# Optimization experiments

Hardware: AMD Instinct MI355X
Metric: run time of the kernel (lower is better)

## Reference

```python
import jax, jax.numpy as jnp
import numpy as np

B, S, H, K = 64, 512, 1024, 7

def setup_inputs() -> dict:
    key = jax.random.key(0)
    ks = jax.random.split(key, 7)
    x = jax.random.normal(ks[0], (B, S, H), dtype=jnp.float32)
    gt = jax.random.randint(ks[1], (B, S), 0, K, dtype=jnp.int64)
    mask = jnp.ones((B, S), dtype=bool)
    # learned parameters
    W = jax.random.normal(ks[2], (H, K), dtype=jnp.float32) * (1.0 / np.sqrt(H))
    b = jnp.zeros((K,), dtype=jnp.float32)
    start_trans = jax.random.uniform(ks[3], (K,), minval=-0.1, maxval=0.1)
    end_trans = jax.random.uniform(ks[4], (K,), minval=-0.1, maxval=0.1)
    trans = jax.random.uniform(ks[5], (K, K), minval=-0.1, maxval=0.1)
    return {"x": x, "gt": gt, "mask": mask, "W": W, "b": b,
            "start_trans": start_trans, "end_trans": end_trans, "trans": trans}

def _crf_neg_llh(emissions, gt, mask, start_trans, end_trans, trans):
    # emissions: [B,S,K], gt: [B,S] int, mask: [B,S] bool
    maskf = mask.astype(emissions.dtype)
    # ---- numerator: score of gold path ----
    em_at_tag = jnp.take_along_axis(emissions, gt[..., None], axis=-1)[..., 0]  # [B,S]
    trans_sc = trans[gt[:, :-1], gt[:, 1:]]                                      # [B,S-1]
    num = start_trans[gt[:, 0]] + em_at_tag[:, 0]
    num = num + jnp.sum((trans_sc + em_at_tag[:, 1:]) * maskf[:, 1:], axis=1)
    last_idx = jnp.sum(mask, axis=1).astype(jnp.int32) - 1                       # [B]
    last_tags = jnp.take_along_axis(gt, last_idx[:, None], axis=1)[:, 0]
    num = num + end_trans[last_tags]
    # ---- denominator: log partition via forward algorithm (lax.scan) ----
    alpha0 = start_trans[None, :] + emissions[:, 0]                              # [B,K]
    em_rest = jnp.transpose(emissions[:, 1:], (1, 0, 2))                         # [S-1,B,K]
    m_rest = jnp.transpose(mask[:, 1:], (1, 0))                                  # [S-1,B]
    def step(alpha, inp):
        em_t, m_t = inp
        nxt = jax.nn.logsumexp(alpha[:, :, None] + trans[None, :, :] + em_t[:, None, :], axis=1)
        return jnp.where(m_t[:, None], nxt, alpha), None
    alpha, _ = jax.lax.scan(step, alpha0, (em_rest, m_rest))
    denom = jax.nn.logsumexp(alpha + end_trans[None, :], axis=1)                 # [B]
    llh = num - denom
    return -jnp.mean(llh)  # reduction='mean', module returns negative

def reference(x, gt, mask, W, b, start_trans, end_trans, trans):
    emissions = jnp.einsum('bsh,hk->bsk', x, W) + b
    return _crf_neg_llh(emissions, gt, mask, start_trans, end_trans, trans)
```

## Files before the change

kernel.cpp:

```cpp
#include <hip/hip_runtime.h>
#include <math.h>

#define NB 64
#define NS 512
#define NH 1024
#define NK 7
#define NCHUNK 16
#define CLEN 32

__global__ __launch_bounds__(256) void emis_kernel(
    const float* __restrict__ x, const float* __restrict__ W,
    const float* __restrict__ bias, float* __restrict__ em, int nrows)
{
    const int lane    = threadIdx.x & 63;
    const int wave_id = blockIdx.x * (blockDim.x >> 6) + (threadIdx.x >> 6);
    const int nwaves  = gridDim.x * (blockDim.x >> 6);

    float w[4][4][NK];
#pragma unroll
    for (int c = 0; c < 4; ++c)
#pragma unroll
        for (int i = 0; i < 4; ++i) {
            const int h = 4 * (c * 64 + lane) + i;
#pragma unroll
            for (int k = 0; k < NK; ++k)
                w[c][i][k] = W[h * NK + k];
        }
    const float bl = bias[lane < NK ? lane : 0];

    for (int row = wave_id; row < nrows; row += nwaves) {
        const float4* xr = (const float4*)(x + (size_t)row * NH);
        float acc[NK];
#pragma unroll
        for (int k = 0; k < NK; ++k) acc[k] = 0.f;
#pragma unroll
        for (int c = 0; c < 4; ++c) {
            const float4 v = xr[c * 64 + lane];
#pragma unroll
            for (int k = 0; k < NK; ++k)
                acc[k] += v.x * w[c][0][k] + v.y * w[c][1][k]
                        + v.z * w[c][2][k] + v.w * w[c][3][k];
        }
#pragma unroll
        for (int m = 1; m < 8; m <<= 1)
#pragma unroll
            for (int k = 0; k < NK; ++k)
                acc[k] += __shfl_xor(acc[k], m, 64);
        const int s = lane & 7;
        const float v01 = (s & 1) ? acc[1] : acc[0];
        const float v23 = (s & 1) ? acc[3] : acc[2];
        const float v45 = (s & 1) ? acc[5] : acc[4];
        const float v67 = acc[6];
        const float w03 = (s & 2) ? v23 : v01;
        const float w47 = (s & 2) ? v67 : v45;
        float v = (s & 4) ? w47 : w03;
        v += __shfl_xor(v, 8, 64);
        v += __shfl_xor(v, 16, 64);
        v += __shfl_xor(v, 32, 64);
        if (lane < NK)
            em[(size_t)row * NK + lane] = v + bl;
    }
}

__global__ __launch_bounds__(64) void chunk_kernel(
    const float* __restrict__ em, const float* __restrict__ trans,
    float* __restrict__ chunkP)
{
    __shared__ float lds_em[CLEN * 8];
    __shared__ float lds_tr[49];
    const int lane = threadIdx.x;
    const int b = blockIdx.x >> 4;
    const int c = blockIdx.x & (NCHUNK - 1);
    const int t0 = c * CLEN;

    if (lane < 49) lds_tr[lane] = trans[lane];
    const float* emb = em + ((size_t)b * NS + t0) * NK;
    for (int idx = lane; idx < CLEN * NK; idx += 64) {
        const int t = idx / NK;
        const int k = idx - t * NK;
        lds_em[t * 8 + k] = emb[idx];
    }
    __syncthreads();

    const int li = lane < 49 ? lane : 48;
    const int i = li / 7;
    const int k = li - i * 7;
    float tj[NK];
#pragma unroll
    for (int j = 0; j < NK; ++j) tj[j] = lds_tr[j * 7 + k];

    const int ts = (c == 0) ? 1 : t0;
    float P = lds_tr[i * 7 + k] + lds_em[(ts - t0) * 8 + k];
    for (int t = ts + 1; t < t0 + CLEN; ++t) {
        float a[NK];
#pragma unroll
        for (int j = 0; j < NK; ++j)
            a[j] = __shfl(P, i * 7 + j, 64) + tj[j];
        const float m = fmaxf(fmaxf(fmaxf(a[0], a[1]), fmaxf(a[2], a[3])),
                              fmaxf(fmaxf(a[4], a[5]), a[6]));
        const float su = __expf(a[0]-m) + __expf(a[1]-m) + __expf(a[2]-m)
                       + __expf(a[3]-m) + __expf(a[4]-m) + __expf(a[5]-m)
                       + __expf(a[6]-m);
        P = m + __logf(su) + lds_em[(t - t0) * 8 + k];
    }
    if (lane < 49)
        chunkP[(size_t)(b * NCHUNK + c) * 49 + lane] = P;
}

__global__ __launch_bounds__(64) void combine_kernel(
    const float* __restrict__ em, const float* __restrict__ chunkP,
    const int* __restrict__ gt32,
    const float* __restrict__ start_trans, const float* __restrict__ end_trans,
    const float* __restrict__ trans, float* __restrict__ llh_out)
{
    __shared__ float lds_C[NCHUNK * 49];
    __shared__ float lds_tr[49];
    __shared__ int   lds_gt[NS];
    const int b    = blockIdx.x;
    const int lane = threadIdx.x;

    int oddbits = 0;
    for (int i = lane; i < 256; i += 64) oddbits |= gt32[2 * i + 1];
    const bool is64 = (__ballot(oddbits != 0) == 0ull);

    for (int idx = lane; idx < NCHUNK * 49; idx += 64)
        lds_C[idx] = chunkP[(size_t)b * NCHUNK * 49 + idx];
    for (int i = lane; i < NS; i += 64) {
        const int gidx = b * NS + i;
        lds_gt[i] = is64 ? gt32[2 * gidx] : gt32[gidx];
    }
    if (lane < 49) lds_tr[lane] = trans[lane];
    __syncthreads();

    const float* emb = em + (size_t)b * NS * NK;
    float numpart = 0.f;
#pragma unroll
    for (int ii = 0; ii < NS / 64; ++ii) {
        const int t = lane + 64 * ii;
        const int g = lds_gt[t];
        if (t == 0) numpart += start_trans[g] + emb[g];
        else        numpart += lds_tr[lds_gt[t - 1] * 7 + g] + emb[t * NK + g];
    }
#pragma unroll
    for (int m = 1; m < 64; m <<= 1) numpart += __shfl_xor(numpart, m, 64);
    const float num = numpart + end_trans[lds_gt[NS - 1]];

    const int kk = lane < NK ? lane : NK - 1;
    float alpha = start_trans[kk] + emb[kk];
#pragma unroll
    for (int c = 0; c < NCHUNK; ++c) {
        float a[NK];
#pragma unroll
        for (int j = 0; j < NK; ++j)
            a[j] = __shfl(alpha, j, 64) + lds_C[c * 49 + j * 7 + kk];
        const float m = fmaxf(fmaxf(fmaxf(a[0], a[1]), fmaxf(a[2], a[3])),
                              fmaxf(fmaxf(a[4], a[5]), a[6]));
        const float su = __expf(a[0]-m) + __expf(a[1]-m) + __expf(a[2]-m)
                       + __expf(a[3]-m) + __expf(a[4]-m) + __expf(a[5]-m)
                       + __expf(a[6]-m);
        alpha = m + __logf(su);
    }

    float v = (lane < NK) ? (alpha + end_trans[kk]) : -3.0e38f;
    float mv = v;
#pragma unroll
    for (int m = 1; m < 8; m <<= 1) mv = fmaxf(mv, __shfl_xor(mv, m, 64));
    float e = (lane < NK) ? __expf(v - mv) : 0.f;
#pragma unroll
    for (int m = 1; m < 8; m <<= 1) e += __shfl_xor(e, m, 64);
    if (lane == 0) llh_out[b] = (mv + __logf(e)) - num;
}

__global__ __launch_bounds__(64) void reduce_kernel(
    const float* __restrict__ llh, float* __restrict__ out)
{
    float v = llh[threadIdx.x];
#pragma unroll
    for (int m = 1; m < 64; m <<= 1) v += __shfl_xor(v, m, 64);
    if (threadIdx.x == 0) out[0] = v * (1.0f / NB);
}

extern "C" void kernel_launch(void* const* d_in, const int* in_sizes, int n_in,
                              void* d_out, int out_size, void* d_ws, size_t ws_size,
                              hipStream_t stream)
{
    const float* x    = (const float*)d_in[0];
    const int*   gt   = (const int*)d_in[1];
    const float* W    = (const float*)d_in[3];
    const float* bias = (const float*)d_in[4];
    const float* st   = (const float*)d_in[5];
    const float* et   = (const float*)d_in[6];
    const float* tr   = (const float*)d_in[7];

    float* em     = (float*)d_ws;
    float* chunkP = em + (size_t)NB * NS * NK;
    float* llh    = chunkP + (size_t)NB * NCHUNK * 49;

    emis_kernel<<<512, 256, 0, stream>>>(x, W, bias, em, NB * NS);
    chunk_kernel<<<NB * NCHUNK, 64, 0, stream>>>(em, tr, chunkP);
    combine_kernel<<<NB, 64, 0, stream>>>(em, chunkP, gt, st, et, tr, llh);
    reduce_kernel<<<1, 64, 0, stream>>>(llh, (float*)d_out);
}
```

Measured before the change: 227.5 us.

## Fuse emission GEMV into chunk scan and fold mean via atomicAdd

```diff
diff --git a/kernel.cpp b/kernel.cpp
--- a/kernel.cpp
+++ b/kernel.cpp
@@ -8,38 +8,47 @@
 #define NCHUNK 16
 #define CLEN 32
 
-__global__ __launch_bounds__(256) void emis_kernel(
+__global__ __launch_bounds__(256) void fused_emis_chunk(
     const float* __restrict__ x, const float* __restrict__ W,
-    const float* __restrict__ bias, float* __restrict__ em, int nrows)
+    const float* __restrict__ bias, const float* __restrict__ trans,
+    float* __restrict__ em, float* __restrict__ chunkP)
 {
-    const int lane    = threadIdx.x & 63;
-    const int wave_id = blockIdx.x * (blockDim.x >> 6) + (threadIdx.x >> 6);
-    const int nwaves  = gridDim.x * (blockDim.x >> 6);
+    __shared__ float lds_em[CLEN * 8];
+    __shared__ float lds_tr[49];
+
+    const int lane = threadIdx.x & 63;
+    const int wave = threadIdx.x >> 6;
+    const int b = blockIdx.x >> 4;
+    const int c = blockIdx.x & (NCHUNK - 1);
+    const int t0 = c * CLEN;
+    const int row0 = b * NS + t0;
+
+    if (threadIdx.x < 49) lds_tr[threadIdx.x] = trans[threadIdx.x];
 
     float w[4][4][NK];
 #pragma unroll
-    for (int c = 0; c < 4; ++c)
+    for (int cc = 0; cc < 4; ++cc)
 #pragma unroll
         for (int i = 0; i < 4; ++i) {
-            const int h = 4 * (c * 64 + lane) + i;
+            const int h = 4 * (cc * 64 + lane) + i;
 #pragma unroll
             for (int k = 0; k < NK; ++k)
-                w[c][i][k] = W[h * NK + k];
+                w[cc][i][k] = W[h * NK + k];
         }
     const float bl = bias[lane < NK ? lane : 0];
 
-    for (int row = wave_id; row < nrows; row += nwaves) {
-        const float4* xr = (const float4*)(x + (size_t)row * NH);
+    for (int r = wave; r < CLEN; r += 4) {
+        const float4* xr = (const float4*)(x + (size_t)(row0 + r) * NH);
         float acc[NK];
 #pragma unroll
         for (int k = 0; k < NK; ++k) acc[k] = 0.f;
 #pragma unroll
-        for (int c = 0; c < 4; ++c) {
-            const float4 v = xr[c * 64 + lane];
+        for (int cc = 0; cc < 4; ++cc) {
+            const float4 v = xr[cc * 64 + lane];
 #pragma unroll
             for (int k = 0; k < NK; ++k)
-                acc[k] += v.x * w[c][0][k] + v.y * w[c][1][k]
-                        + v.z * w[c][2][k] + v.w * w[c][3][k];
+                acc[k] += v.x * w[cc][0][k] + v.y * w[cc][1][k]
+                        + v.z * w[cc][2][k] + v.w * w[cc][3][k];
         }
 #pragma unroll
         for (int m = 1; m < 8; m <<= 1)
@@ -50,37 +59,20 @@
         const float v01 = (s & 1) ? acc[1] : acc[0];
         const float v23 = (s & 1) ? acc[3] : acc[2];
         const float v45 = (s & 1) ? acc[5] : acc[4];
-        const float v67 = acc[6];
         const float w03 = (s & 2) ? v23 : v01;
-        const float w47 = (s & 2) ? v67 : v45;
+        const float w47 = (s & 2) ? acc[6] : v45;
         float v = (s & 4) ? w47 : w03;
         v += __shfl_xor(v, 8, 64);
         v += __shfl_xor(v, 16, 64);
         v += __shfl_xor(v, 32, 64);
-        if (lane < NK)
-            em[(size_t)row * NK + lane] = v + bl;
-    }
-}
-
-__global__ __launch_bounds__(64) void chunk_kernel(
-    const float* __restrict__ em, const float* __restrict__ trans,
-    float* __restrict__ chunkP)
-{
-    __shared__ float lds_em[CLEN * 8];
-    __shared__ float lds_tr[49];
-    const int lane = threadIdx.x;
-    const int b = blockIdx.x >> 4;
-    const int c = blockIdx.x & (NCHUNK - 1);
-    const int t0 = c * CLEN;
-
-    if (lane < 49) lds_tr[lane] = trans[lane];
-    const float* emb = em + ((size_t)b * NS + t0) * NK;
-    for (int idx = lane; idx < CLEN * NK; idx += 64) {
-        const int t = idx / NK;
-        const int k = idx - t * NK;
-        lds_em[t * 8 + k] = emb[idx];
+        if (lane < NK) {
+            const float e = v + bl;
+            lds_em[r * 8 + lane] = e;
+            em[(size_t)(row0 + r) * NK + lane] = e;
+        }
     }
     __syncthreads();
+    if (wave != 0) return;
 
     const int li = lane < 49 ? lane : 48;
     const int i = li / 7;
@@ -89,9 +81,9 @@
 #pragma unroll
     for (int j = 0; j < NK; ++j) tj[j] = lds_tr[j * 7 + k];
 
-    const int ts = (c == 0) ? 1 : t0;
-    float P = lds_tr[i * 7 + k] + lds_em[(ts - t0) * 8 + k];
-    for (int t = ts + 1; t < t0 + CLEN; ++t) {
+    const int first = (c == 0) ? 1 : 0;
+    float P = lds_tr[i * 7 + k] + lds_em[first * 8 + k];
+    for (int t = first + 1; t < CLEN; ++t) {
         float a[NK];
 #pragma unroll
         for (int j = 0; j < NK; ++j)
@@ -101,7 +93,7 @@
         const float su = __expf(a[0]-m) + __expf(a[1]-m) + __expf(a[2]-m)
                        + __expf(a[3]-m) + __expf(a[4]-m) + __expf(a[5]-m)
                        + __expf(a[6]-m);
-        P = m + __logf(su) + lds_em[(t - t0) * 8 + k];
+        P = m + __logf(su) + lds_em[t * 8 + k];
     }
     if (lane < 49)
         chunkP[(size_t)(b * NCHUNK + c) * 49 + lane] = P;
@@ -111,7 +103,7 @@
     const float* __restrict__ em, const float* __restrict__ chunkP,
     const int* __restrict__ gt32,
     const float* __restrict__ start_trans, const float* __restrict__ end_trans,
-    const float* __restrict__ trans, float* __restrict__ llh_out)
+    const float* __restrict__ trans, float* __restrict__ out)
 {
     __shared__ float lds_C[NCHUNK * 49];
     __shared__ float lds_tr[49];
@@ -168,16 +160,8 @@
     float e = (lane < NK) ? __expf(v - mv) : 0.f;
 #pragma unroll
     for (int m = 1; m < 8; m <<= 1) e += __shfl_xor(e, m, 64);
-    if (lane == 0) llh_out[b] = (mv + __logf(e)) - num;
-}
-
-__global__ __launch_bounds__(64) void reduce_kernel(
-    const float* __restrict__ llh, float* __restrict__ out)
-{
-    float v = llh[threadIdx.x];
-#pragma unroll
-    for (int m = 1; m < 64; m <<= 1) v += __shfl_xor(v, m, 64);
-    if (threadIdx.x == 0) out[0] = v * (1.0f / NB);
+    if (lane == 0)
+        atomicAdd(out, ((mv + __logf(e)) - num) * (1.0f / NB));
 }
 
 extern "C" void kernel_launch(void* const* d_in, const int* in_sizes, int n_in,
@@ -194,10 +178,8 @@
 
     float* em     = (float*)d_ws;
     float* chunkP = em + (size_t)NB * NS * NK;
-    float* llh    = chunkP + (size_t)NB * NCHUNK * 49;
 
-    emis_kernel<<<512, 256, 0, stream>>>(x, W, bias, em, NB * NS);
-    chunk_kernel<<<NB * NCHUNK, 64, 0, stream>>>(em, tr, chunkP);
-    combine_kernel<<<NB, 64, 0, stream>>>(em, chunkP, gt, st, et, tr, llh);
-    reduce_kernel<<<1, 64, 0, stream>>>(llh, (float*)d_out);
+    hipMemsetAsync(d_out, 0, sizeof(float) * out_size, stream);
+    fused_emis_chunk<<<NB * NCHUNK, 256, 0, stream>>>(x, W, bias, tr, em, chunkP);
+    combine_kernel<<<NB, 64, 0, stream>>>(em, chunkP, gt, st, et, tr, (float*)d_out);
 }
```

Result: no change. 227.0 us (-0.2%).
